# Optimization experiments

Hardware: AMD Instinct MI355X
Metric: run time of the kernel (lower is better)

Reference implementation:

```python
import jax, jax.numpy as jnp
import numpy as np


def _rope(x):
    # x: [..., T, hs]
    T, hs = x.shape[-2], x.shape[-1]
    pos = jnp.arange(T, dtype=x.dtype)[:, None]                      # [T,1]
    theta = 1.0 / (10000.0 ** (jnp.arange(0, hs, 2, dtype=x.dtype) / hs))  # [hs/2]
    ang = pos * theta                                                # [T, hs/2]
    cos, sin = jnp.cos(ang), jnp.sin(ang)
    x1, x2 = x[..., 0::2], x[..., 1::2]
    out = jnp.stack([x1 * cos - x2 * sin, x1 * sin + x2 * cos], axis=-1)
    return out.reshape(x.shape)


def _layernorm(x, w, b, eps=1e-5):
    mu = jnp.mean(x, axis=-1, keepdims=True)
    var = jnp.mean(jnp.square(x - mu), axis=-1, keepdims=True)
    return (x - mu) * jax.lax.rsqrt(var + eps) * w + b


def setup_inputs() -> dict:
    key = jax.random.key(0)
    ks = jax.random.split(key, 8)
    B, T, D, H, HS = 8, 1024, 1024, 16, 64
    s = lambda fan: 1.0 / np.sqrt(fan)
    return {
        'x': jax.random.normal(ks[0], (B, T, D), jnp.float32),
        'wq': jax.random.normal(ks[1], (H, D, HS), jnp.float32) * s(D),
        'wk': jax.random.normal(ks[2], (H, D, HS), jnp.float32) * s(D),
        'wv': jax.random.normal(ks[3], (H, D, HS), jnp.float32) * s(D),
        'w_proj': jax.random.normal(ks[4], (D, D), jnp.float32) * s(D),
        'b_proj': jnp.zeros((D,), jnp.float32),
        'ln1_w': jnp.ones((D,), jnp.float32),
        'ln1_b': jnp.zeros((D,), jnp.float32),
        'ln2_w': jnp.ones((D,), jnp.float32),
        'ln2_b': jnp.zeros((D,), jnp.float32),
        'w1': jax.random.normal(ks[5], (D, 4 * D), jnp.float32) * s(D),
        'b1': jnp.zeros((4 * D,), jnp.float32),
        'w2': jax.random.normal(ks[6], (4 * D, D), jnp.float32) * s(4 * D),
        'b2': jnp.zeros((D,), jnp.float32),
    }


def reference(x, wq, wk, wv, w_proj, b_proj, ln1_w, ln1_b, ln2_w, ln2_b, w1, b1, w2, b2):
    B, T, D = x.shape
    H, _, HS = wq.shape
    # --- attention sub-block (pre-LN, causal, RoPE on q/k) ---
    xn = _layernorm(x, ln1_w, ln1_b)
    q = jnp.einsum('btd,hdk->bhtk', xn, wq)   # [B,H,T,HS]
    k = jnp.einsum('btd,hdk->bhtk', xn, wk)
    v = jnp.einsum('btd,hdk->bhtk', xn, wv)
    q = _rope(q)
    k = _rope(k)
    scores = jnp.einsum('bhqk,bhsk->bhqs', q, k) * (HS ** -0.5)  # [B,H,T,T]
    causal = jnp.tril(jnp.ones((T, T), bool))
    scores = jnp.where(causal, scores, -jnp.inf)
    attn = jax.nn.softmax(scores, axis=-1)
    o = jnp.einsum('bhqs,bhsk->bhqk', attn, v)                   # [B,H,T,HS]
    o = jnp.transpose(o, (0, 2, 1, 3)).reshape(B, T, H * HS)     # concat heads
    x = x + o @ w_proj + b_proj                                  # dropout is identity in eval
    # --- FFN sub-block ---
    xn2 = _layernorm(x, ln2_w, ln2_b)
    h = jax.nn.relu(xn2 @ w1 + b1)
    x = x + h @ w2 + b2
    return x
```

## Files before the change

kernel.cpp:

```cpp
#include <hip/hip_runtime.h>
#include <hip/hip_bf16.h>
#include <math.h>

#define DEV static __device__ __forceinline__

typedef __attribute__((ext_vector_type(8))) __bf16 bf16x8;
typedef __attribute__((ext_vector_type(4))) float f32x4;
typedef __attribute__((ext_vector_type(8))) unsigned short ushort8;
typedef __attribute__((ext_vector_type(4))) unsigned short ushort4v;

#define Bb 8
#define Tt 1024
#define Dd 1024
#define Hh 16
#define HS 64
#define BT 8192
#define DFF 4096
#define QS 8388608ull

DEV unsigned short f2bf(float f) {
  union { float f; unsigned int u; } v; v.f = f;
  unsigned int r = v.u + 0x7fffu + ((v.u >> 16) & 1u);
  return (unsigned short)(r >> 16);
}
DEV float bf2f(unsigned short h) {
  union { unsigned int u; float f; } v; v.u = ((unsigned int)h) << 16;
  return v.f;
}

DEV void gload_lds16(const void* g, void* l) {
  __builtin_amdgcn_global_load_lds(
      (const __attribute__((address_space(1))) void*)g,
      (__attribute__((address_space(3))) void*)l, 16, 0, 0);
}

__global__ __launch_bounds__(256) void pack_qkv_t(const float* __restrict__ wq,
                                                  const float* __restrict__ wk,
                                                  const float* __restrict__ wv,
                                                  unsigned short* __restrict__ dst) {
  __shared__ float tile[32][33];
  int z = blockIdx.z, which = z >> 4, hh = z & 15;
  const float* src = which == 0 ? wq : (which == 1 ? wk : wv);
  int d0 = blockIdx.y * 32, hs0 = blockIdx.x * 32;
  int c = threadIdx.x & 31, r8 = threadIdx.x >> 5;
  #pragma unroll
  for (int r = 0; r < 4; ++r) {
    int d = d0 + r8 + r * 8;
    tile[r8 + r * 8][c] = src[((size_t)hh * Dd + d) * HS + hs0 + c];
  }
  __syncthreads();
  #pragma unroll
  for (int r = 0; r < 4; ++r) {
    int hs = hs0 + r8 + r * 8;
    dst[((size_t)which * 1024 + hh * 64 + hs) * Dd + d0 + c] = f2bf(tile[c][r8 + r * 8]);
  }
}

__global__ __launch_bounds__(256) void pack_t_tiled(const float* __restrict__ src,
                                                    unsigned short* __restrict__ dst,
                                                    int N, int K) {
  __shared__ float tile[32][33];
  int n0 = blockIdx.x * 32, k0 = blockIdx.y * 32;
  int c = threadIdx.x & 31, r8 = threadIdx.x >> 5;
  #pragma unroll
  for (int r = 0; r < 4; ++r)
    tile[r8 + r * 8][c] = src[(size_t)(k0 + r8 + r * 8) * N + n0 + c];
  __syncthreads();
  #pragma unroll
  for (int r = 0; r < 4; ++r)
    dst[(size_t)(n0 + r8 + r * 8) * K + k0 + c] = f2bf(tile[c][r8 + r * 8]);
}

__global__ __launch_bounds__(256) void ln_k(const float* __restrict__ in,
                                            const float* __restrict__ w,
                                            const float* __restrict__ b,
                                            unsigned short* __restrict__ out) {
  __shared__ float sbuf[8];
  int row = blockIdx.x, t = threadIdx.x;
  const float4 v = ((const float4*)(in + (size_t)row * Dd))[t];
  float s = v.x + v.y + v.z + v.w;
  float q = v.x * v.x + v.y * v.y + v.z * v.z + v.w * v.w;
  #pragma unroll
  for (int o = 32; o > 0; o >>= 1) { s += __shfl_down(s, o); q += __shfl_down(q, o); }
  if ((t & 63) == 0) { sbuf[t >> 6] = s; sbuf[4 + (t >> 6)] = q; }
  __syncthreads();
  s = (sbuf[0] + sbuf[1]) + (sbuf[2] + sbuf[3]);
  q = (sbuf[4] + sbuf[5]) + (sbuf[6] + sbuf[7]);
  float mu = s * (1.f / Dd);
  float var = q * (1.f / Dd) - mu * mu;
  float inv = rsqrtf(var + 1e-5f);
  const float4 wv = ((const float4*)w)[t];
  const float4 bv = ((const float4*)b)[t];
  ushort4v r;
  r[0] = f2bf((v.x - mu) * inv * wv.x + bv.x);
  r[1] = f2bf((v.y - mu) * inv * wv.y + bv.y);
  r[2] = f2bf((v.z - mu) * inv * wv.z + bv.z);
  r[3] = f2bf((v.w - mu) * inv * wv.w + bv.w);
  *(ushort4v*)&out[(size_t)row * Dd + t * 4] = r;
}

template <bool ISA>
DEV void stage_half(const unsigned short* __restrict__ gbase, int ldK, int k0,
                    unsigned short* lbase, int half, int tid) {
  #pragma unroll
  for (int j = 0; j < 2; ++j) {
    int idx = j * 512 + tid;
    int lr = half * 128 + (idx >> 3);
    int slot = idx & 7;
    int g;
    if (ISA) g = ((lr >> 6) & 1) * 128 + ((lr >> 7) & 1) * 64 + (lr & 63);
    else     g = ((lr >> 5) & 3) * 64  + ((lr >> 7) & 1) * 32 + (lr & 31);
    const unsigned short* src = gbase + (size_t)g * ldK + k0 + ((slot ^ (lr & 7)) * 8);
    gload_lds16(src, lbase + (size_t)half * 8192 + (size_t)idx * 8);
  }
}

template <int MODE>
__global__ __launch_bounds__(512, 2) void gemm256_k(
    const unsigned short* __restrict__ A, const unsigned short* __restrict__ Bt,
    int M, int N, int K,
    const float* __restrict__ bias, unsigned short* __restrict__ outb) {
  __shared__ __align__(16) unsigned short lds_all[4][16384];
  const int tid = threadIdx.x;
  const int lane = tid & 63;
  const int wave = tid >> 6;
  const int l15 = lane & 15, lg = lane >> 4;
  const int wm = wave >> 2, wn = wave & 3;
  const int sw = l15 & 7;

  int nwg = gridDim.x * gridDim.y;
  int orig = blockIdx.y * gridDim.x + blockIdx.x;
  int swz = (orig & 7) * (nwg >> 3) + (orig >> 3);
  int bx = swz % gridDim.x, by = swz / gridDim.x;
  const int brow = by * 256, bcol = bx * 256;

  const unsigned short* Ag = A + (size_t)brow * K;
  const unsigned short* Bg = Bt + (size_t)bcol * K;
  const int NT = K >> 6;

  stage_half<true >(Ag, K, 0, lds_all[0], 0, tid);
  stage_half<true >(Ag, K, 0, lds_all[0], 1, tid);
  stage_half<false>(Bg, K, 0, lds_all[1], 0, tid);
  stage_half<false>(Bg, K, 0, lds_all[1], 1, tid);
  stage_half<true >(Ag, K, 64, lds_all[2], 0, tid);
  stage_half<false>(Bg, K, 64, lds_all[3], 0, tid);
  stage_half<true >(Ag, K, 64, lds_all[2], 1, tid);
  asm volatile("s_waitcnt vmcnt(6)" ::: "memory");
  __builtin_amdgcn_s_barrier();

  f32x4 acc[8][4] = {};
  bf16x8 af[4][2], bfr[4][2];

  for (int t = 0; t < NT; ++t) {
    const unsigned short* At  = lds_all[(t & 1) * 2 + 0];
    const unsigned short* Btl = lds_all[(t & 1) * 2 + 1];
    unsigned short* Bn = lds_all[((t & 1) ^ 1) * 2 + 1];
    unsigned short* Ac = (unsigned short*)At;
    unsigned short* Bc = (unsigned short*)Btl;

    #pragma unroll
    for (int mi = 0; mi < 4; ++mi) {
      int lr = wm * 64 + mi * 16 + l15;
      #pragma unroll
      for (int kk = 0; kk < 2; ++kk)
        af[mi][kk] = *(const bf16x8*)&At[(size_t)lr * 64 + (((kk * 4 + lg) ^ sw) * 8)];
    }
    #pragma unroll
    for (int ni = 0; ni < 2; ++ni) {
      int lr = wn * 32 + ni * 16 + l15;
      #pragma unroll
      for (int kk = 0; kk < 2; ++kk)
        bfr[ni][kk] = *(const bf16x8*)&Btl[(size_t)lr * 64 + (((kk * 4 + lg) ^ sw) * 8)];
    }
    if (t + 1 < NT) stage_half<false>(Bg, K, (t + 1) * 64, Bn, 1, tid);
    __builtin_amdgcn_s_barrier();
    asm volatile("s_waitcnt lgkmcnt(0)" ::: "memory");
    __builtin_amdgcn_sched_barrier(0);
    __builtin_amdgcn_s_setprio(1);
    #pragma unroll
    for (int kk = 0; kk < 2; ++kk)
      #pragma unroll
      for (int mi = 0; mi < 4; ++mi)
        #pragma unroll
        for (int ni = 0; ni < 2; ++ni)
          acc[mi][ni] = __builtin_amdgcn_mfma_f32_16x16x32_bf16(af[mi][kk], bfr[ni][kk], acc[mi][ni], 0, 0, 0);
    __builtin_amdgcn_s_setprio(0);
    __builtin_amdgcn_s_barrier();

    #pragma unroll
    for (int ni = 2; ni < 4; ++ni) {
      int lr = 128 + wn * 32 + (ni & 1) * 16 + l15;
      #pragma unroll
      for (int kk = 0; kk < 2; ++kk)
        bfr[ni][kk] = *(const bf16x8*)&Btl[(size_t)lr * 64 + (((kk * 4 + lg) ^ sw) * 8)];
    }
    if (t + 2 < NT) stage_half<true>(Ag, K, (t + 2) * 64, Ac, 0, tid);
    __builtin_amdgcn_s_barrier();
    asm volatile("s_waitcnt lgkmcnt(0)" ::: "memory");
    __builtin_amdgcn_sched_barrier(0);
    __builtin_amdgcn_s_setprio(1);
    #pragma unroll
    for (int kk = 0; kk < 2; ++kk)
      #pragma unroll
      for (int mi = 0; mi < 4; ++mi)
        #pragma unroll
        for (int ni = 2; ni < 4; ++ni)
          acc[mi][ni] = __builtin_amdgcn_mfma_f32_16x16x32_bf16(af[mi][kk], bfr[ni][kk], acc[mi][ni], 0, 0, 0);
    __builtin_amdgcn_s_setprio(0);
    __builtin_amdgcn_s_barrier();

    #pragma unroll
    for (int mi = 0; mi < 4; ++mi) {
      int lr = 128 + wm * 64 + mi * 16 + l15;
      #pragma unroll
      for (int kk = 0; kk < 2; ++kk)
        af[mi][kk] = *(const bf16x8*)&At[(size_t)lr * 64 + (((kk * 4 + lg) ^ sw) * 8)];
    }
    if (t + 2 < NT) stage_half<false>(Bg, K, (t + 2) * 64, Bc, 0, tid);
    __builtin_amdgcn_s_barrier();
    asm volatile("s_waitcnt lgkmcnt(0)" ::: "memory");
    __builtin_amdgcn_sched_barrier(0);
    __builtin_amdgcn_s_setprio(1);
    #pragma unroll
    for (int kk = 0; kk < 2; ++kk)
      #pragma unroll
      for (int mi = 0; mi < 4; ++mi)
        #pragma unroll
        for (int ni = 0; ni < 2; ++ni)
          acc[4 + mi][ni] = __builtin_amdgcn_mfma_f32_16x16x32_bf16(af[mi][kk], bfr[ni][kk], acc[4 + mi][ni], 0, 0, 0);
    __builtin_amdgcn_s_setprio(0);
    __builtin_amdgcn_s_barrier();

    if (t + 2 < NT) {
      stage_half<true>(Ag, K, (t + 2) * 64, Ac, 1, tid);
      asm volatile("s_waitcnt vmcnt(6)" ::: "memory");
    } else if (t + 1 < NT) {
      asm volatile("s_waitcnt vmcnt(0)" ::: "memory");
    }
    __builtin_amdgcn_s_barrier();
    __builtin_amdgcn_s_setprio(1);
    #pragma unroll
    for (int kk = 0; kk < 2; ++kk)
      #pragma unroll
      for (int mi = 0; mi < 4; ++mi)
        #pragma unroll
        for (int ni = 2; ni < 4; ++ni)
          acc[4 + mi][ni] = __builtin_amdgcn_mfma_f32_16x16x32_bf16(af[mi][kk], bfr[ni][kk], acc[4 + mi][ni], 0, 0, 0);
    __builtin_amdgcn_s_setprio(0);
    __builtin_amdgcn_s_barrier();
  }

  #pragma unroll
  for (int m = 0; m < 8; ++m) {
    #pragma unroll
    for (int n = 0; n < 4; ++n) {
      int row0 = brow + wm * 128 + m * 16 + lg * 4;
      int col = bcol + wn * 64 + n * 16 + l15;
      if constexpr (MODE == 0) {
        int b = row0 >> 10, t0 = row0 & 1023;
        int which = col >> 10, rem = col & 1023, hh = rem >> 6, hs = rem & 63;
        if (which == 2) {
          uint2 pk;
          pk.x = (unsigned int)f2bf(acc[m][n][0]) | ((unsigned int)f2bf(acc[m][n][1]) << 16);
          pk.y = (unsigned int)f2bf(acc[m][n][2]) | ((unsigned int)f2bf(acc[m][n][3]) << 16);
          *(uint2*)&outb[2 * QS + ((size_t)(b * Hh + hh) * HS + hs) * Tt + t0] = pk;
        } else {
          float theta = exp2f(-(float)(hs >> 1) * 0.4152410118609203f);
          float qs = (which == 0) ? 0.18033688f : 1.0f;
          float sgn = ((hs & 1) == 0) ? -1.0f : 1.0f;
          #pragma unroll
          for (int r = 0; r < 4; ++r) {
            float own = acc[m][n][r];
            float partner = __shfl_xor(own, 1);
            float sn, cs;
            __sincosf((float)(t0 + r) * theta, &sn, &cs);
            float val = (cs * own + sgn * sn * partner) * qs;
            outb[(size_t)which * QS + ((size_t)((b * Hh + hh) * Tt + t0 + r)) * HS + hs] =
                f2bf(val);
          }
        }
      } else {
        #pragma unroll
        for (int r = 0; r < 4; ++r) {
          float z = acc[m][n][r] + bias[col];
          outb[(size_t)(row0 + r) * N + col] = f2bf(z > 0.f ? z : 0.f);
        }
      }
    }
  }
}

DEV void stage_A128(const unsigned short* __restrict__ Ag, int ldK, int k0,
                    unsigned short* abuf, int half, int tid) {
  int lr = half * 64 + (tid >> 3);
  int slot = tid & 7;
  int g = ((lr >> 5) & 1) * 64 + ((lr >> 6) & 1) * 32 + (lr & 31);
  gload_lds16(Ag + (size_t)g * ldK + k0 + ((slot ^ (lr & 7)) * 8),
              abuf + (size_t)half * 4096 + (size_t)tid * 8);
}

__global__ __launch_bounds__(512, 2) void gemm128_k(
    const unsigned short* __restrict__ A, const unsigned short* __restrict__ Bt,
    int M, int N, int K,
    const float* __restrict__ resid, const float* __restrict__ bias,
    float* __restrict__ outf) {
  __shared__ __align__(16) unsigned short ldsA[2][8192];
  __shared__ __align__(16) unsigned short ldsB[2][16384];
  const int tid = threadIdx.x;
  const int lane = tid & 63;
  const int wave = tid >> 6;
  const int l15 = lane & 15, lg = lane >> 4;
  const int wm = wave >> 2, wn = wave & 3;
  const int sw = l15 & 7;

  int nwg = gridDim.x * gridDim.y;
  int orig = blockIdx.y * gridDim.x + blockIdx.x;
  int swz = (orig & 7) * (nwg >> 3) + (orig >> 3);
  int bx = swz % gridDim.x, by = swz / gridDim.x;
  const int brow = by * 128, bcol = bx * 256;

  const unsigned short* Ag = A + (size_t)brow * K;
  const unsigned short* Bg = Bt + (size_t)bcol * K;
  const int NT = K >> 6;

  stage_A128(Ag, K, 0, ldsA[0], 0, tid);
  stage_A128(Ag, K, 0, ldsA[0], 1, tid);
  stage_half<false>(Bg, K, 0, ldsB[0], 0, tid);
  stage_half<false>(Bg, K, 0, ldsB[0], 1, tid);
  stage_A128(Ag, K, 64, ldsA[1], 0, tid);
  stage_half<false>(Bg, K, 64, ldsB[1], 0, tid);
  stage_A128(Ag, K, 64, ldsA[1], 1, tid);
  asm volatile("s_waitcnt vmcnt(4)" ::: "memory");
  __builtin_amdgcn_s_barrier();

  f32x4 acc[4][4] = {};
  bf16x8 af[2][2], bfr[4][2];

  for (int t = 0; t < NT; ++t) {
    const unsigned short* At  = ldsA[t & 1];
    const unsigned short* Btl = ldsB[t & 1];
    unsigned short* Bn = ldsB[(t & 1) ^ 1];
    unsigned short* Ac = (unsigned short*)At;
    unsigned short* Bc = (unsigned short*)Btl;

    #pragma unroll
    for (int mi = 0; mi < 2; ++mi) {
      int lr = wm * 32 + mi * 16 + l15;
      #pragma unroll
      for (int kk = 0; kk < 2; ++kk)
        af[mi][kk] = *(const bf16x8*)&At[(size_t)lr * 64 + (((kk * 4 + lg) ^ sw) * 8)];
    }
    #pragma unroll
    for (int ni = 0; ni < 2; ++ni) {
      int lr = wn * 32 + ni * 16 + l15;
      #pragma unroll
      for (int kk = 0; kk < 2; ++kk)
        bfr[ni][kk] = *(const bf16x8*)&Btl[(size_t)lr * 64 + (((kk * 4 + lg) ^ sw) * 8)];
    }
    if (t + 1 < NT) stage_half<false>(Bg, K, (t + 1) * 64, Bn, 1, tid);
    __builtin_amdgcn_s_barrier();
    asm volatile("s_waitcnt lgkmcnt(0)" ::: "memory");
    __builtin_amdgcn_sched_barrier(0);
    __builtin_amdgcn_s_setprio(1);
    #pragma unroll
    for (int kk = 0; kk < 2; ++kk)
      #pragma unroll
      for (int mi = 0; mi < 2; ++mi)
        #pragma unroll
        for (int ni = 0; ni < 2; ++ni)
          acc[mi][ni] = __builtin_amdgcn_mfma_f32_16x16x32_bf16(af[mi][kk], bfr[ni][kk], acc[mi][ni], 0, 0, 0);
    __builtin_amdgcn_s_setprio(0);
    __builtin_amdgcn_s_barrier();

    #pragma unroll
    for (int ni = 2; ni < 4; ++ni) {
      int lr = 128 + wn * 32 + (ni & 1) * 16 + l15;
      #pragma unroll
      for (int kk = 0; kk < 2; ++kk)
        bfr[ni][kk] = *(const bf16x8*)&Btl[(size_t)lr * 64 + (((kk * 4 + lg) ^ sw) * 8)];
    }
    if (t + 2 < NT) stage_A128(Ag, K, (t + 2) * 64, Ac, 0, tid);
    __builtin_amdgcn_s_barrier();
    asm volatile("s_waitcnt lgkmcnt(0)" ::: "memory");
    __builtin_amdgcn_sched_barrier(0);
    __builtin_amdgcn_s_setprio(1);
    #pragma unroll
    for (int kk = 0; kk < 2; ++kk)
      #pragma unroll
      for (int mi = 0; mi < 2; ++mi)
        #pragma unroll
        for (int ni = 2; ni < 4; ++ni)
          acc[mi][ni] = __builtin_amdgcn_mfma_f32_16x16x32_bf16(af[mi][kk], bfr[ni][kk], acc[mi][ni], 0, 0, 0);
    __builtin_amdgcn_s_setprio(0);
    __builtin_amdgcn_s_barrier();

    #pragma unroll
    for (int mi = 0; mi < 2; ++mi) {
      int lr = 64 + wm * 32 + mi * 16 + l15;
      #pragma unroll
      for (int kk = 0; kk < 2; ++kk)
        af[mi][kk] = *(const bf16x8*)&At[(size_t)lr * 64 + (((kk * 4 + lg) ^ sw) * 8)];
    }
    if (t + 2 < NT) stage_half<false>(Bg, K, (t + 2) * 64, Bc, 0, tid);
    __builtin_amdgcn_s_barrier();
    asm volatile("s_waitcnt lgkmcnt(0)" ::: "memory");
    __builtin_amdgcn_sched_barrier(0);
    __builtin_amdgcn_s_setprio(1);
    #pragma unroll
    for (int kk = 0; kk < 2; ++kk)
      #pragma unroll
      for (int mi = 0; mi < 2; ++mi)
        #pragma unroll
        for (int ni = 0; ni < 2; ++ni)
          acc[2 + mi][ni] = __builtin_amdgcn_mfma_f32_16x16x32_bf16(af[mi][kk], bfr[ni][kk], acc[2 + mi][ni], 0, 0, 0);
    __builtin_amdgcn_s_setprio(0);
    __builtin_amdgcn_s_barrier();

    if (t + 2 < NT) {
      stage_A128(Ag, K, (t + 2) * 64, Ac, 1, tid);
      asm volatile("s_waitcnt vmcnt(4)" ::: "memory");
    } else if (t + 1 < NT) {
      asm volatile("s_waitcnt vmcnt(0)" ::: "memory");
    }
    __builtin_amdgcn_s_barrier();
    __builtin_amdgcn_s_setprio(1);
    #pragma unroll
    for (int kk = 0; kk < 2; ++kk)
      #pragma unroll
      for (int mi = 0; mi < 2; ++mi)
        #pragma unroll
        for (int ni = 2; ni < 4; ++ni)
          acc[2 + mi][ni] = __builtin_amdgcn_mfma_f32_16x16x32_bf16(af[mi][kk], bfr[ni][kk], acc[2 + mi][ni], 0, 0, 0);
    __builtin_amdgcn_s_setprio(0);
    __builtin_amdgcn_s_barrier();
  }

  #pragma unroll
  for (int m = 0; m < 4; ++m) {
    #pragma unroll
    for (int n = 0; n < 4; ++n) {
      int row0 = brow + wm * 64 + m * 16 + lg * 4;
      int col = bcol + wn * 64 + n * 16 + l15;
      #pragma unroll
      for (int r = 0; r < 4; ++r)
        outf[(size_t)(row0 + r) * N + col] =
            resid[(size_t)(row0 + r) * N + col] + acc[m][n][r] + bias[col];
    }
  }
}

__global__ __launch_bounds__(256) void attn_k(const unsigned short* __restrict__ qkv,
                                              unsigned short* __restrict__ O) {
  __shared__ __align__(16) unsigned short K_lds[2][64 * 64];
  __shared__ __align__(16) unsigned short Vt_lds[2][64 * 64];
  __shared__ __align__(16) unsigned short P_lds[4][32 * 64];
  const int tid = threadIdx.x;
  const int wave = tid >> 6, lane = tid & 63;
  const int l15 = lane & 15, lg = lane >> 4;
  const int sw = l15 & 7;
  const int bh = blockIdx.x;
  const int q0 = (7 - (int)blockIdx.y) * 128;
  const int qw0 = q0 + wave * 32;

  bf16x8 qf[2][2];
  {
    const unsigned short* Qg = qkv + ((size_t)bh * Tt + qw0 + l15) * HS;
    #pragma unroll
    for (int qi = 0; qi < 2; ++qi)
      #pragma unroll
      for (int dg = 0; dg < 2; ++dg)
        qf[qi][dg] = *(const bf16x8*)&Qg[(size_t)qi * 16 * HS + dg * 32 + lg * 8];
  }
  f32x4 oacc[2][4] = {};
  float m_r[2] = {-1e30f, -1e30f};
  float l_r[2] = {0.f, 0.f};

  const unsigned short* Kg = qkv + QS + (size_t)bh * Tt * HS;
  const unsigned short* Vg = qkv + 2 * QS + (size_t)bh * HS * Tt;

  const int srow = lane >> 3;
  const int scol = ((lane & 7) ^ (srow & 7)) * 8;
  const int i0 = wave * 2, i1 = wave * 2 + 1;

#define STAGE_KV(s0_, buf_)                                                        \
  do {                                                                             \
    gload_lds16(Kg + (size_t)((s0_) + i0 * 8 + srow) * HS + scol,                  \
                (char*)&K_lds[buf_][0] + i0 * 1024);                               \
    gload_lds16(Kg + (size_t)((s0_) + i1 * 8 + srow) * HS + scol,                  \
                (char*)&K_lds[buf_][0] + i1 * 1024);                               \
    gload_lds16(Vg + (size_t)(i0 * 8 + srow) * Tt + (s0_) + scol,                  \
                (char*)&Vt_lds[buf_][0] + i0 * 1024);                              \
    gload_lds16(Vg + (size_t)(i1 * 8 + srow) * Tt + (s0_) + scol,                  \
                (char*)&Vt_lds[buf_][0] + i1 * 1024);                              \
  } while (0)

  const int nsteps = (q0 + 128) >> 6;
  STAGE_KV(0, 0);

  for (int t = 0; t < nsteps; ++t) {
    const int s0 = t << 6;
    if (t + 1 < nsteps) {
      STAGE_KV(s0 + 64, (t + 1) & 1);
      asm volatile("s_waitcnt vmcnt(4)" ::: "memory");
    } else {
      asm volatile("s_waitcnt vmcnt(0)" ::: "memory");
    }
    __builtin_amdgcn_s_barrier();

    const unsigned short* Kb = K_lds[t & 1];
    const unsigned short* Vb = Vt_lds[t & 1];

    if (s0 <= qw0 + 31) {
      f32x4 st[4][2];
      #pragma unroll
      for (int si = 0; si < 4; ++si) {
        bf16x8 kf0 = *(const bf16x8*)&Kb[(size_t)(si * 16 + l15) * 64 + ((lg ^ sw) * 8)];
        bf16x8 kf1 = *(const bf16x8*)&Kb[(size_t)(si * 16 + l15) * 64 + (((4 + lg) ^ sw) * 8)];
        #pragma unroll
        for (int qi = 0; qi < 2; ++qi) {
          f32x4 a = {};
          a = __builtin_amdgcn_mfma_f32_16x16x32_bf16(kf0, qf[qi][0], a, 0, 0, 0);
          a = __builtin_amdgcn_mfma_f32_16x16x32_bf16(kf1, qf[qi][1], a, 0, 0, 0);
          st[si][qi] = a;
        }
      }
      if (s0 + 63 > qw0) {
        #pragma unroll
        for (int si = 0; si < 4; ++si)
          #pragma unroll
          for (int qi = 0; qi < 2; ++qi) {
            int base = (s0 + si * 16 + lg * 4) - (qw0 + qi * 16 + l15);
            #pragma unroll
            for (int r = 0; r < 4; ++r)
              if (base + r > 0) st[si][qi][r] = -1e30f;
          }
      }
      #pragma unroll
      for (int qi = 0; qi < 2; ++qi) {
        float ms[4];
        #pragma unroll
        for (int si = 0; si < 4; ++si)
          ms[si] = fmaxf(fmaxf(st[si][qi][0], st[si][qi][1]),
                         fmaxf(st[si][qi][2], st[si][qi][3]));
        float pm = fmaxf(fmaxf(ms[0], ms[1]), fmaxf(ms[2], ms[3]));
        pm = fmaxf(pm, __shfl_xor(pm, 16));
        pm = fmaxf(pm, __shfl_xor(pm, 32));
        if (__any(pm - m_r[qi] > 8.f)) {
          float mn = fmaxf(m_r[qi], pm);
          float corr = __builtin_amdgcn_exp2f(m_r[qi] - mn);
          m_r[qi] = mn;
          l_r[qi] *= corr;
          #pragma unroll
          for (int r = 0; r < 4; ++r) {
            float c = __shfl(corr, (lane & 48) + lg * 4 + r);
            #pragma unroll
            for (int dj = 0; dj < 4; ++dj) oacc[qi][dj][r] *= c;
          }
        }
        float rs = 0.f;
        #pragma unroll
        for (int si = 0; si < 4; ++si) {
          #pragma unroll
          for (int r = 0; r < 4; ++r) {
            float p = __builtin_amdgcn_exp2f(st[si][qi][r] - m_r[qi]);
            st[si][qi][r] = p;
            rs += p;
          }
        }
        rs += __shfl_xor(rs, 16);
        rs += __shfl_xor(rs, 32);
        l_r[qi] += rs;
        #pragma unroll
        for (int si = 0; si < 4; ++si) {
          uint2 pk;
          asm("v_cvt_pk_bf16_f32 %0, %1, %2"
              : "=v"(pk.x) : "v"(st[si][qi][0]), "v"(st[si][qi][1]));
          asm("v_cvt_pk_bf16_f32 %0, %1, %2"
              : "=v"(pk.y) : "v"(st[si][qi][2]), "v"(st[si][qi][3]));
          int slot = si * 2 + (lg >> 1);
          *(uint2*)&P_lds[wave][(size_t)(qi * 16 + l15) * 64 + ((slot ^ sw) * 8) + (lg & 1) * 4] = pk;
        }
      }
      bf16x8 pf[2][2];
      #pragma unroll
      for (int qi = 0; qi < 2; ++qi)
        #pragma unroll
        for (int sg = 0; sg < 2; ++sg)
          pf[qi][sg] = *(const bf16x8*)&P_lds[wave][(size_t)(qi * 16 + l15) * 64 + (((sg * 4 + lg) ^ sw) * 8)];
      #pragma unroll
      for (int dj = 0; dj < 4; ++dj) {
        bf16x8 vf0 = *(const bf16x8*)&Vb[(size_t)(dj * 16 + l15) * 64 + ((lg ^ sw) * 8)];
        bf16x8 vf1 = *(const bf16x8*)&Vb[(size_t)(dj * 16 + l15) * 64 + (((4 + lg) ^ sw) * 8)];
        #pragma unroll
        for (int qi = 0; qi < 2; ++qi) {
          oacc[qi][dj] = __builtin_amdgcn_mfma_f32_16x16x32_bf16(pf[qi][0], vf0, oacc[qi][dj], 0, 0, 0);
          oacc[qi][dj] = __builtin_amdgcn_mfma_f32_16x16x32_bf16(pf[qi][1], vf1, oacc[qi][dj], 0, 0, 0);
        }
      }
    }
    __builtin_amdgcn_s_barrier();
  }
#undef STAGE_KV

  int b = bh >> 4, hh = bh & 15;
  #pragma unroll
  for (int qi = 0; qi < 2; ++qi) {
    float linv = 1.f / l_r[qi];
    #pragma unroll
    for (int r = 0; r < 4; ++r) {
      float li = __shfl(linv, (lane & 48) + lg * 4 + r);
      int qg = qw0 + qi * 16 + lg * 4 + r;
      unsigned short* Og = O + ((size_t)(b * Tt + qg)) * Dd + hh * HS;
      #pragma unroll
      for (int dj = 0; dj < 4; ++dj)
        Og[dj * 16 + l15] = f2bf(oacc[qi][dj][r] * li);
    }
  }
}

extern "C" void kernel_launch(void* const* d_in, const int* in_sizes, int n_in,
                              void* d_out, int out_size, void* d_ws, size_t ws_size,
                              hipStream_t stream) {
  const float* x      = (const float*)d_in[0];
  const float* wq     = (const float*)d_in[1];
  const float* wk     = (const float*)d_in[2];
  const float* wv     = (const float*)d_in[3];
  const float* w_proj = (const float*)d_in[4];
  const float* b_proj = (const float*)d_in[5];
  const float* ln1_w  = (const float*)d_in[6];
  const float* ln1_b  = (const float*)d_in[7];
  const float* ln2_w  = (const float*)d_in[8];
  const float* ln2_b  = (const float*)d_in[9];
  const float* w1     = (const float*)d_in[10];
  const float* b1     = (const float*)d_in[11];
  const float* w2     = (const float*)d_in[12];
  const float* b2     = (const float*)d_in[13];
  float* out = (float*)d_out;

  char* ws = (char*)d_ws;
  unsigned short* Wt_qkv  = (unsigned short*)(ws + 0);
  unsigned short* Wt_proj = (unsigned short*)(ws + 6291456);
  unsigned short* Wt_1    = (unsigned short*)(ws + 8388608);
  unsigned short* Wt_2    = (unsigned short*)(ws + 16777216);
  float*          x1      = (float*)(ws + 25165824);
  unsigned short* xn      = (unsigned short*)(ws + 58720256);
  unsigned short* qkv     = (unsigned short*)(ws + 75497472);
  unsigned short* O       = (unsigned short*)(ws + 125829120);
  unsigned short* xn2     = O;
  unsigned short* hbuf    = (unsigned short*)(ws + 58720256);

  pack_qkv_t<<<dim3(2, 32, 48), 256, 0, stream>>>(wq, wk, wv, Wt_qkv);
  pack_t_tiled<<<dim3(32, 32), 256, 0, stream>>>(w_proj, Wt_proj, 1024, 1024);
  pack_t_tiled<<<dim3(128, 32), 256, 0, stream>>>(w1, Wt_1, 4096, 1024);
  pack_t_tiled<<<dim3(32, 128), 256, 0, stream>>>(w2, Wt_2, 1024, 4096);

  ln_k<<<BT, 256, 0, stream>>>(x, ln1_w, ln1_b, xn);

  gemm256_k<0><<<dim3(12, 32), 512, 0, stream>>>(xn, Wt_qkv, BT, 3072, 1024,
                                                 nullptr, qkv);

  attn_k<<<dim3(128, 8), 256, 0, stream>>>(qkv, O);

  gemm128_k<<<dim3(4, 64), 512, 0, stream>>>(O, Wt_proj, BT, 1024, 1024,
                                             x, b_proj, x1);
  ln_k<<<BT, 256, 0, stream>>>(x1, ln2_w, ln2_b, xn2);

  gemm256_k<2><<<dim3(16, 32), 512, 0, stream>>>(xn2, Wt_1, BT, 4096, 1024,
                                                 b1, hbuf);
  gemm128_k<<<dim3(4, 64), 512, 0, stream>>>(hbuf, Wt_2, BT, 1024, 4096,
                                             x1, b2, out);
}
```

Before: 346.6 us.

## Split-K the FFN down-projection with atomics and precompute RoPE cos/sin table

The final FFN GEMM (K=4096) now runs on the 256x256 gemm kernel with a split-K of 2 across gridDim.z. Partial sums are combined with float atomic adds into an output prefilled with residual plus bias by a new elementwise kernel. Separately, RoPE sin/cos values are precomputed once into a table and read in the QKV epilogue instead of computing sincos per element. This raises parallelism for the down-projection but adds atomic traffic, an extra pass over the output, and nondeterministic summation order.

```diff
diff --git a/kernel.cpp b/kernel.cpp
--- a/kernel.cpp
+++ b/kernel.cpp
@@ -32,6 +32,24 @@
   __builtin_amdgcn_global_load_lds(
       (const __attribute__((address_space(1))) void*)g,
       (__attribute__((address_space(3))) void*)l, 16, 0, 0);
+}
+
+__global__ void rope_tab_k(float2* __restrict__ tab) {
+  int idx = blockIdx.x * 256 + threadIdx.x;
+  int t = idx >> 5, i = idx & 31;
+  float theta = exp2f(-(float)i * (13.287712379549449f / 32.f));
+  float sn, cs;
+  sincosf((float)t * theta, &sn, &cs);
+  tab[idx] = make_float2(cs, sn);
+}
+
+__global__ void prefill_k(const float* __restrict__ x1, const float* __restrict__ b2,
+                          float* __restrict__ out) {
+  int i = blockIdx.x * 256 + threadIdx.x;
+  float4 v = ((const float4*)x1)[i];
+  float4 b = ((const float4*)b2)[i & 255];
+  v.x += b.x; v.y += b.y; v.z += b.z; v.w += b.w;
+  ((float4*)out)[i] = v;
 }
 
 __global__ __launch_bounds__(256) void pack_qkv_t(const float* __restrict__ wq,
@@ -119,7 +137,8 @@
 __global__ __launch_bounds__(512, 2) void gemm256_k(
     const unsigned short* __restrict__ A, const unsigned short* __restrict__ Bt,
     int M, int N, int K,
-    const float* __restrict__ bias, unsigned short* __restrict__ outb) {
+    const float* __restrict__ bias, unsigned short* __restrict__ outb,
+    float* __restrict__ outf) {
   __shared__ __align__(16) unsigned short lds_all[4][16384];
   const int tid = threadIdx.x;
   const int lane = tid & 63;
@@ -134,17 +153,20 @@
   int bx = swz % gridDim.x, by = swz / gridDim.x;
   const int brow = by * 256, bcol = bx * 256;
 
+  const int Keff = K / (int)gridDim.z;
+  const int koff = (int)blockIdx.z * Keff;
+
   const unsigned short* Ag = A + (size_t)brow * K;
   const unsigned short* Bg = Bt + (size_t)bcol * K;
-  const int NT = K >> 6;
-
-  stage_half<true >(Ag, K, 0, lds_all[0], 0, tid);
-  stage_half<true >(Ag, K, 0, lds_all[0], 1, tid);
-  stage_half<false>(Bg, K, 0, lds_all[1], 0, tid);
-  stage_half<false>(Bg, K, 0, lds_all[1], 1, tid);
-  stage_half<true >(Ag, K, 64, lds_all[2], 0, tid);
-  stage_half<false>(Bg, K, 64, lds_all[3], 0, tid);
-  stage_half<true >(Ag, K, 64, lds_all[2], 1, tid);
+  const int NT = Keff >> 6;
+
+  stage_half<true >(Ag, K, koff, lds_all[0], 0, tid);
+  stage_half<true >(Ag, K, koff, lds_all[0], 1, tid);
+  stage_half<false>(Bg, K, koff, lds_all[1], 0, tid);
+  stage_half<false>(Bg, K, koff, lds_all[1], 1, tid);
+  stage_half<true >(Ag, K, koff + 64, lds_all[2], 0, tid);
+  stage_half<false>(Bg, K, koff + 64, lds_all[3], 0, tid);
+  stage_half<true >(Ag, K, koff + 64, lds_all[2], 1, tid);
   asm volatile("s_waitcnt vmcnt(6)" ::: "memory");
   __builtin_amdgcn_s_barrier();
 
@@ -172,7 +194,7 @@
       for (int kk = 0; kk < 2; ++kk)
         bfr[ni][kk] = *(const bf16x8*)&Btl[(size_t)lr * 64 + (((kk * 4 + lg) ^ sw) * 8)];
     }
-    if (t + 1 < NT) stage_half<false>(Bg, K, (t + 1) * 64, Bn, 1, tid);
+    if (t + 1 < NT) stage_half<false>(Bg, K, koff + (t + 1) * 64, Bn, 1, tid);
     __builtin_amdgcn_s_barrier();
     asm volatile("s_waitcnt lgkmcnt(0)" ::: "memory");
     __builtin_amdgcn_sched_barrier(0);
@@ -194,7 +216,7 @@
       for (int kk = 0; kk < 2; ++kk)
         bfr[ni][kk] = *(const bf16x8*)&Btl[(size_t)lr * 64 + (((kk * 4 + lg) ^ sw) * 8)];
     }
-    if (t + 2 < NT) stage_half<true>(Ag, K, (t + 2) * 64, Ac, 0, tid);
+    if (t + 2 < NT) stage_half<true>(Ag, K, koff + (t + 2) * 64, Ac, 0, tid);
     __builtin_amdgcn_s_barrier();
     asm volatile("s_waitcnt lgkmcnt(0)" ::: "memory");
     __builtin_amdgcn_sched_barrier(0);
@@ -216,7 +238,7 @@
       for (int kk = 0; kk < 2; ++kk)
         af[mi][kk] = *(const bf16x8*)&At[(size_t)lr * 64 + (((kk * 4 + lg) ^ sw) * 8)];
     }
-    if (t + 2 < NT) stage_half<false>(Bg, K, (t + 2) * 64, Bc, 0, tid);
+    if (t + 2 < NT) stage_half<false>(Bg, K, koff + (t + 2) * 64, Bc, 0, tid);
     __builtin_amdgcn_s_barrier();
     asm volatile("s_waitcnt lgkmcnt(0)" ::: "memory");
     __builtin_amdgcn_sched_barrier(0);
@@ -232,7 +254,7 @@
     __builtin_amdgcn_s_barrier();
 
     if (t + 2 < NT) {
-      stage_half<true>(Ag, K, (t + 2) * 64, Ac, 1, tid);
+      stage_half<true>(Ag, K, koff + (t + 2) * 64, Ac, 1, tid);
       asm volatile("s_waitcnt vmcnt(6)" ::: "memory");
     } else if (t + 1 < NT) {
       asm volatile("s_waitcnt vmcnt(0)" ::: "memory");
@@ -265,26 +287,29 @@
           pk.y = (unsigned int)f2bf(acc[m][n][2]) | ((unsigned int)f2bf(acc[m][n][3]) << 16);
           *(uint2*)&outb[2 * QS + ((size_t)(b * Hh + hh) * HS + hs) * Tt + t0] = pk;
         } else {
-          float theta = exp2f(-(float)(hs >> 1) * 0.4152410118609203f);
+          const float2* tab = (const float2*)bias;
           float qs = (which == 0) ? 0.18033688f : 1.0f;
           float sgn = ((hs & 1) == 0) ? -1.0f : 1.0f;
           #pragma unroll
           for (int r = 0; r < 4; ++r) {
             float own = acc[m][n][r];
             float partner = __shfl_xor(own, 1);
-            float sn, cs;
-            __sincosf((float)(t0 + r) * theta, &sn, &cs);
-            float val = (cs * own + sgn * sn * partner) * qs;
+            float2 cssn = tab[(size_t)(t0 + r) * 32 + (hs >> 1)];
+            float val = (cssn.x * own + sgn * cssn.y * partner) * qs;
             outb[(size_t)which * QS + ((size_t)((b * Hh + hh) * Tt + t0 + r)) * HS + hs] =
                 f2bf(val);
           }
         }
-      } else {
+      } else if constexpr (MODE == 2) {
         #pragma unroll
         for (int r = 0; r < 4; ++r) {
           float z = acc[m][n][r] + bias[col];
           outb[(size_t)(row0 + r) * N + col] = f2bf(z > 0.f ? z : 0.f);
         }
+      } else {
+        #pragma unroll
+        for (int r = 0; r < 4; ++r)
+          unsafeAtomicAdd(&outf[(size_t)(row0 + r) * N + col], acc[m][n][r]);
       }
     }
   }
@@ -642,6 +667,7 @@
   unsigned short* Wt_proj = (unsigned short*)(ws + 6291456);
   unsigned short* Wt_1    = (unsigned short*)(ws + 8388608);
   unsigned short* Wt_2    = (unsigned short*)(ws + 16777216);
+  float*          rtab    = (float*)(ws + 25165824 - 262144);
   float*          x1      = (float*)(ws + 25165824);
   unsigned short* xn      = (unsigned short*)(ws + 58720256);
   unsigned short* qkv     = (unsigned short*)(ws + 75497472);
@@ -649,6 +675,9 @@
   unsigned short* xn2     = O;
   unsigned short* hbuf    = (unsigned short*)(ws + 58720256);
 
+  rtab = (float*)(ws + 141557760);
+
+  rope_tab_k<<<128, 256, 0, stream>>>((float2*)rtab);
   pack_qkv_t<<<dim3(2, 32, 48), 256, 0, stream>>>(wq, wk, wv, Wt_qkv);
   pack_t_tiled<<<dim3(32, 32), 256, 0, stream>>>(w_proj, Wt_proj, 1024, 1024);
   pack_t_tiled<<<dim3(128, 32), 256, 0, stream>>>(w1, Wt_1, 4096, 1024);
@@ -657,7 +686,7 @@
   ln_k<<<BT, 256, 0, stream>>>(x, ln1_w, ln1_b, xn);
 
   gemm256_k<0><<<dim3(12, 32), 512, 0, stream>>>(xn, Wt_qkv, BT, 3072, 1024,
-                                                 nullptr, qkv);
+                                                 rtab, qkv, nullptr);
 
   attn_k<<<dim3(128, 8), 256, 0, stream>>>(qkv, O);
 
@@ -666,7 +695,9 @@
   ln_k<<<BT, 256, 0, stream>>>(x1, ln2_w, ln2_b, xn2);
 
   gemm256_k<2><<<dim3(16, 32), 512, 0, stream>>>(xn2, Wt_1, BT, 4096, 1024,
-                                                 b1, hbuf);
-  gemm128_k<<<dim3(4, 64), 512, 0, stream>>>(hbuf, Wt_2, BT, 1024, 4096,
-                                             x1, b2, out);
-}
+                                                 b1, hbuf, nullptr);
+
+  prefill_k<<<8192, 256, 0, stream>>>(x1, b2, out);
+  gemm256_k<3><<<dim3(4, 32, 2), 512, 0, stream>>>(hbuf, Wt_2, BT, 1024, 4096,
+                                                   nullptr, nullptr, out);
+}
```

Result: slower. 380.7 us (+9.8%).
